# Kernel tuning notes

Measured on AMD Instinct MI355X. Metric: run time of the kernel, lower is better.

Reference implementation:

```python
import jax, jax.numpy as jnp
import numpy as np
from jax import lax

B, IN_CH, H, W = 512, 20, 32, 32
FEAT, NUM_AGENTS, NUM_ACTIONS = 128, 4, 16
NUM_UNIT, NUM_CITY = 12, 4


def setup_inputs() -> dict:
    key = jax.random.key(0)
    ks = jax.random.split(key, 6)
    states = jax.random.normal(ks[0], (B, IN_CH, H, W), dtype=jnp.float32)
    labels = jax.random.randint(ks[1], (B,), 0, NUM_AGENTS, dtype=jnp.int32)
    maskings = jnp.ones((B, 1, H, W), dtype=jnp.float32)
    # get_feature params: 3x3 conv trunk (stand-in for PolicyNetwork.get_feature)
    conv_w = jax.random.normal(ks[2], (FEAT, IN_CH, 3, 3), dtype=jnp.float32) * 0.05
    conv_b = jnp.zeros((FEAT,), dtype=jnp.float32)
    # Stacked per-agent heads: index 0 = policy_net.fc1, 1.. = fc_list
    W_all = jax.random.normal(ks[3], (NUM_AGENTS, NUM_ACTIONS, FEAT), dtype=jnp.float32) * 0.05
    b_all = jax.random.normal(ks[4], (NUM_AGENTS, NUM_ACTIONS), dtype=jnp.float32) * 0.05
    return {"states": states, "labels": labels, "maskings": maskings,
            "conv_w": conv_w, "conv_b": conv_b, "W_all": W_all, "b_all": b_all}


def _get_feature(states, maskings, conv_w, conv_b):
    x = lax.conv_general_dilated(states, conv_w, (1, 1), 'SAME',
                                 dimension_numbers=('NCHW', 'OIHW', 'NCHW'))
    x = jax.nn.relu(x + conv_b[None, :, None, None])
    return x * maskings  # [B, FEAT, H, W]


def reference(states, labels, maskings, conv_w, conv_b, W_all, b_all):
    x = _get_feature(states, maskings, conv_w, conv_b)
    b, c, h, w = x.shape
    x = x.transpose(0, 2, 3, 1).reshape(b, h * w, c)  # [B, HW, C]
    # Equivalent to computing all num_agents heads then gathering by label:
    # select each sample's head weights, then one batched GEMM.
    W_sel = W_all[labels]          # [B, K, C]
    b_sel = b_all[labels]          # [B, K]
    out = jnp.einsum('bnc,bkc->bnk', x, W_sel) + b_sel[:, None, :]
    out = out.reshape(b, h, w, NUM_ACTIONS)
    return out[..., :NUM_UNIT], out[..., NUM_UNIT:]
```

## Files before the change

kernel.cpp:

```cpp
#include <hip/hip_runtime.h>
#include <hip/hip_bf16.h>
#include <stdint.h>

#define BATCH   512
#define INCH    20
#define FEAT    128
#define KACT    16
#define NUNIT   12

typedef short bf16x8 __attribute__((ext_vector_type(8)));
typedef float f32x4  __attribute__((ext_vector_type(4)));

#define BPACK_ELEMS (3*2*4*128*8)
#define WHEAD_ELEMS (4*4*4*16*8)

#define XIN_ROWS  10
#define XIN_ELEMS (XIN_ROWS*34*20 + 64)

__device__ __forceinline__ uint16_t f2bf(float f) {
    union { float f; uint32_t u; } x{f};
    uint32_t u = x.u;
    return (uint16_t)((u + 0x7FFFu + ((u >> 16) & 1u)) >> 16);
}

__device__ __forceinline__ uint32_t cvt_pk_bf16(float lo, float hi) {
    uint32_t r;
    asm("v_cvt_pk_bf16_f32 %0, %1, %2" : "=v"(r) : "v"(lo), "v"(hi));
    return r;
}

__device__ __forceinline__ void lds_barrier() {
    asm volatile("s_waitcnt lgkmcnt(0)\n\ts_barrier" ::: "memory");
}

__global__ void repack_kernel(const float* __restrict__ conv_w,
                              const float* __restrict__ W_all,
                              uint16_t* __restrict__ Bpack,
                              uint16_t* __restrict__ Whead) {
    int idx = blockIdx.x * 256 + threadIdx.x;
    if (idx < BPACK_ELEMS) {
        int j = idx & 7, t = idx >> 3;
        int f = t & 127; t >>= 7;
        int g = t & 3;   t >>= 2;
        int kk = t & 1;  int ky = t >> 1;
        int k = kk * 32 + g * 8 + j;
        float v = 0.0f;
        if (k < 60) {
            int kx = k / 20, c = k % 20;
            v = conv_w[((f * INCH + c) * 3 + ky) * 3 + kx];
        }
        Bpack[idx] = f2bf(v);
    } else if (idx < BPACK_ELEMS + WHEAD_ELEMS) {
        int i = idx - BPACK_ELEMS;
        int j = i & 7, t = i >> 3;
        int a = t & 15; t >>= 4;
        int g = t & 3;  t >>= 2;
        int kt = t & 3; int ag = t >> 2;
        int f = kt * 32 + g * 8 + j;
        Whead[i] = f2bf(W_all[(ag * KACT + a) * FEAT + f]);
    }
}

__global__ __launch_bounds__(256, 4) void fused_mfma_kernel(
    const float* __restrict__ states,
    const int*   __restrict__ labels,
    const float* __restrict__ maskings,
    const float* __restrict__ conv_b,
    const float* __restrict__ b_all,
    const uint16_t* __restrict__ Bpack,
    const uint16_t* __restrict__ Whead,
    float*       __restrict__ out)
{
    __shared__ __align__(16) uint16_t xin[XIN_ELEMS];
    __shared__ __align__(16) uint16_t xl[2 * 32 * 128];

    const int bid  = blockIdx.x;
    const int b    = bid >> 2;
    const int y0   = (bid & 3) << 3;
    const int tid  = threadIdx.x;
    const int lane = tid & 63;
    const int fq   = tid >> 6;
    const int l15  = lane & 15;
    const int g    = lane >> 4;
    const int swz  = (l15 & 7) << 4;

    for (int i = tid; i < (XIN_ELEMS * 2) / 16; i += 256)
        ((uint4*)xin)[i] = uint4{0, 0, 0, 0};
    __syncthreads();

    for (int t = 0; t < 7; ++t) {
        int i = t * 256 + tid;
        if (i < XIN_ROWS * 5 * 32) {
            int p  = i & 31;
            int tt = i >> 5;
            int cg = tt % 5;
            int r  = tt / 5;
            int y  = y0 + r - 1;
            if (y >= 0 && y < 32) {
                const float* sp = states + (size_t)b * (INCH * 1024) + cg * 4096 + y * 32 + p;
                float v0 = sp[0], v1 = sp[1024], v2 = sp[2048], v3 = sp[3072];
                uint64_t lo = cvt_pk_bf16(v0, v1);
                uint64_t hi = cvt_pk_bf16(v2, v3);
                *(uint64_t*)&xin[(r * 34 + p + 1) * 20 + cg * 4] = lo | (hi << 32);
            }
        }
    }

    const int label = labels[b];
    f32x4 cb[2];
    #pragma unroll
    for (int nt = 0; nt < 2; ++nt)
        cb[nt] = *(const f32x4*)&conv_b[fq * 32 + nt * 16 + g * 4];
    const f32x4 hb = *(const f32x4*)&b_all[label * KACT + g * 4];
    bf16x8 Wh[4];
    #pragma unroll
    for (int kt = 0; kt < 4; ++kt)
        Wh[kt] = *(const bf16x8*)&Whead[(((label * 4 + kt) * 4 + g) * 16 + l15) * 8];

    bf16x8 Wc[3][2][2];
    #pragma unroll
    for (int ky = 0; ky < 3; ++ky)
        #pragma unroll
        for (int kk = 0; kk < 2; ++kk)
            #pragma unroll
            for (int nt = 0; nt < 2; ++nt)
                Wc[ky][kk][nt] = *(const bf16x8*)
                    &Bpack[((((ky * 2 + kk) * 4 + g) * 128 + fq * 32 + nt * 16 + l15) * 8)];

    const int hoff0 = (fq * 16 + l15) * 256;
    const bool do_head = (fq < 2);

    __syncthreads();

    #pragma unroll 2
    for (int s = 0; s < 8; ++s) {
        const int y = y0 + s;

        const float m0 = maskings[(size_t)b * 1024 + y * 32 + l15];
        const float m1 = maskings[(size_t)b * 1024 + y * 32 + 16 + l15];

        f32x4 acc[2][2];
        #pragma unroll
        for (int pt = 0; pt < 2; ++pt)
            #pragma unroll
            for (int nt = 0; nt < 2; ++nt)
                acc[pt][nt] = f32x4{0.f, 0.f, 0.f, 0.f};

        __builtin_amdgcn_s_setprio(1);
        #pragma unroll
        for (int ky = 0; ky < 3; ++ky) {
            const uint64_t* a0 = (const uint64_t*)&xin[((s + ky) * 34 + l15) * 20 + g * 8];
            const uint64_t* a1 = (const uint64_t*)&xin[((s + ky) * 34 + 16 + l15) * 20 + g * 8];
            #pragma unroll
            for (int kk = 0; kk < 2; ++kk) {
                union { uint64_t u[2]; bf16x8 v; } B0, B1;
                B0.u[0] = a0[kk * 8 + 0]; B0.u[1] = a0[kk * 8 + 1];
                B1.u[0] = a1[kk * 8 + 0]; B1.u[1] = a1[kk * 8 + 1];
                #pragma unroll
                for (int nt = 0; nt < 2; ++nt) {
                    acc[0][nt] = __builtin_amdgcn_mfma_f32_16x16x32_bf16(
                        Wc[ky][kk][nt], B0.v, acc[0][nt], 0, 0, 0);
                    acc[1][nt] = __builtin_amdgcn_mfma_f32_16x16x32_bf16(
                        Wc[ky][kk][nt], B1.v, acc[1][nt], 0, 0, 0);
                }
            }
        }
        __builtin_amdgcn_s_setprio(0);

        char* xbase = (char*)xl + (s & 1) * 8192;
        #pragma unroll
        for (int pt = 0; pt < 2; ++pt) {
            const float m = pt ? m1 : m0;
            #pragma unroll
            for (int nt = 0; nt < 2; ++nt) {
                float x0 = fmaxf(acc[pt][nt][0] + cb[nt][0], 0.f) * m;
                float x1 = fmaxf(acc[pt][nt][1] + cb[nt][1], 0.f) * m;
                float x2 = fmaxf(acc[pt][nt][2] + cb[nt][2], 0.f) * m;
                float x3 = fmaxf(acc[pt][nt][3] + cb[nt][3], 0.f) * m;
                uint64_t pk = (uint64_t)cvt_pk_bf16(x0, x1)
                            | ((uint64_t)cvt_pk_bf16(x2, x3) << 32);
                const int off = (pt * 16 + l15) * 256 + fq * 64 + nt * 32 + g * 8;
                *(uint64_t*)(xbase + (off ^ swz)) = pk;
            }
        }

        lds_barrier();

        if (do_head) {
            f32x4 hacc = f32x4{0.f, 0.f, 0.f, 0.f};
            __builtin_amdgcn_s_setprio(1);
            #pragma unroll
            for (int kt = 0; kt < 4; ++kt) {
                const int off = hoff0 + kt * 64 + g * 16;
                bf16x8 bx = *(const bf16x8*)(xbase + (off ^ swz));
                hacc = __builtin_amdgcn_mfma_f32_16x16x32_bf16(Wh[kt], bx, hacc, 0, 0, 0);
            }
            __builtin_amdgcn_s_setprio(0);
            const size_t pos = (size_t)b * 1024 + y * 32 + fq * 16 + l15;
            f32x4 o = hacc + hb;
            if (g < 3) *(f32x4*)&out[pos * NUNIT + g * 4] = o;
            else       *(f32x4*)&out[(size_t)BATCH * 1024 * NUNIT + pos * 4] = o;
        }
    }
}

extern "C" void kernel_launch(void* const* d_in, const int* in_sizes, int n_in,
                              void* d_out, int out_size, void* d_ws, size_t ws_size,
                              hipStream_t stream) {
    const float* states   = (const float*)d_in[0];
    const int*   labels   = (const int*)d_in[1];
    const float* maskings = (const float*)d_in[2];
    const float* conv_w   = (const float*)d_in[3];
    const float* conv_b   = (const float*)d_in[4];
    const float* W_all    = (const float*)d_in[5];
    const float* b_all    = (const float*)d_in[6];
    float* out = (float*)d_out;

    uint16_t* Bpack = (uint16_t*)d_ws;
    uint16_t* Whead = Bpack + BPACK_ELEMS;

    repack_kernel<<<(BPACK_ELEMS + WHEAD_ELEMS + 255) / 256, 256, 0, stream>>>(
        conv_w, W_all, Bpack, Whead);
    fused_mfma_kernel<<<BATCH * 4, 256, 0, stream>>>(
        states, labels, maskings, conv_b, b_all, Bpack, Whead, out);
}
```

Before: 42.15 us.

## Process two output rows per iteration to reuse input row loads across ky taps

New measurement: 42.62 us. No clear change (+1.1%).

```diff
diff --git a/kernel.cpp b/kernel.cpp
--- a/kernel.cpp
+++ b/kernel.cpp
@@ -61,7 +61,7 @@
     }
 }
 
-__global__ __launch_bounds__(256, 4) void fused_mfma_kernel(
+__global__ __launch_bounds__(256, 3) void fused_mfma_kernel(
     const float* __restrict__ states,
     const int*   __restrict__ labels,
     const float* __restrict__ maskings,
@@ -72,7 +72,7 @@
     float*       __restrict__ out)
 {
     __shared__ __align__(16) uint16_t xin[XIN_ELEMS];
-    __shared__ __align__(16) uint16_t xl[2 * 32 * 128];
+    __shared__ __align__(16) uint16_t xl[2 * 64 * 128];
 
     const int bid  = blockIdx.x;
     const int b    = bid >> 2;
@@ -128,65 +128,74 @@
                     &Bpack[((((ky * 2 + kk) * 4 + g) * 128 + fq * 32 + nt * 16 + l15) * 8)];
 
     const int hoff0 = (fq * 16 + l15) * 256;
-    const bool do_head = (fq < 2);
 
     __syncthreads();
 
     #pragma unroll 2
-    for (int s = 0; s < 8; ++s) {
-        const int y = y0 + s;
-
-        const float m0 = maskings[(size_t)b * 1024 + y * 32 + l15];
-        const float m1 = maskings[(size_t)b * 1024 + y * 32 + 16 + l15];
-
-        f32x4 acc[2][2];
+    for (int s = 0; s < 4; ++s) {
+        float mk[2][2];
         #pragma unroll
-        for (int pt = 0; pt < 2; ++pt)
-            #pragma unroll
-            for (int nt = 0; nt < 2; ++nt)
-                acc[pt][nt] = f32x4{0.f, 0.f, 0.f, 0.f};
+        for (int rr = 0; rr < 2; ++rr)
+            #pragma unroll
+            for (int pt = 0; pt < 2; ++pt)
+                mk[rr][pt] = maskings[(size_t)b * 1024 + (y0 + 2 * s + rr) * 32 + pt * 16 + l15];
+
+        char* xbase = (char*)xl + (s & 1) * 16384;
 
         __builtin_amdgcn_s_setprio(1);
         #pragma unroll
-        for (int ky = 0; ky < 3; ++ky) {
-            const uint64_t* a0 = (const uint64_t*)&xin[((s + ky) * 34 + l15) * 20 + g * 8];
-            const uint64_t* a1 = (const uint64_t*)&xin[((s + ky) * 34 + 16 + l15) * 20 + g * 8];
-            #pragma unroll
-            for (int kk = 0; kk < 2; ++kk) {
-                union { uint64_t u[2]; bf16x8 v; } B0, B1;
-                B0.u[0] = a0[kk * 8 + 0]; B0.u[1] = a0[kk * 8 + 1];
-                B1.u[0] = a1[kk * 8 + 0]; B1.u[1] = a1[kk * 8 + 1];
+        for (int pt = 0; pt < 2; ++pt) {
+            f32x4 a0[2], a1[2];
+            #pragma unroll
+            for (int nt = 0; nt < 2; ++nt) {
+                a0[nt] = f32x4{0.f, 0.f, 0.f, 0.f};
+                a1[nt] = f32x4{0.f, 0.f, 0.f, 0.f};
+            }
+
+            #pragma unroll
+            for (int t = 0; t < 4; ++t) {
+                const uint64_t* ap = (const uint64_t*)
+                    &xin[((2 * s + t) * 34 + pt * 16 + l15) * 20 + g * 8];
+                union { uint64_t u[2]; bf16x8 v; } X0, X1;
+                X0.u[0] = ap[0]; X0.u[1] = ap[1];
+                X1.u[0] = ap[8]; X1.u[1] = ap[9];
+                #pragma unroll
+                for (int kk = 0; kk < 2; ++kk) {
+                    const bf16x8 Xk = kk ? X1.v : X0.v;
+                    #pragma unroll
+                    for (int nt = 0; nt < 2; ++nt) {
+                        if (t < 3)
+                            a0[nt] = __builtin_amdgcn_mfma_f32_16x16x32_bf16(
+                                Wc[t][kk][nt], Xk, a0[nt], 0, 0, 0);
+                        if (t > 0)
+                            a1[nt] = __builtin_amdgcn_mfma_f32_16x16x32_bf16(
+                                Wc[t - 1][kk][nt], Xk, a1[nt], 0, 0, 0);
+                    }
+                }
+            }
+
+            #pragma unroll
+            for (int rr = 0; rr < 2; ++rr) {
+                const float m = mk[rr][pt];
                 #pragma unroll
                 for (int nt = 0; nt < 2; ++nt) {
-                    acc[0][nt] = __builtin_amdgcn_mfma_f32_16x16x32_bf16(
-                        Wc[ky][kk][nt], B0.v, acc[0][nt], 0, 0, 0);
-                    acc[1][nt] = __builtin_amdgcn_mfma_f32_16x16x32_bf16(
-                        Wc[ky][kk][nt], B1.v, acc[1][nt], 0, 0, 0);
+                    const f32x4 A = rr ? a1[nt] : a0[nt];
+                    float x0 = fmaxf(A[0] + cb[nt][0], 0.f) * m;
+                    float x1 = fmaxf(A[1] + cb[nt][1], 0.f) * m;
+                    float x2 = fmaxf(A[2] + cb[nt][2], 0.f) * m;
+                    float x3 = fmaxf(A[3] + cb[nt][3], 0.f) * m;
+                    uint64_t pk = (uint64_t)cvt_pk_bf16(x0, x1)
+                                | ((uint64_t)cvt_pk_bf16(x2, x3) << 32);
+                    const int off = ((rr * 2 + pt) * 16 + l15) * 256 + fq * 64 + nt * 32 + g * 8;
+                    *(uint64_t*)(xbase + (off ^ swz)) = pk;
                 }
             }
         }
         __builtin_amdgcn_s_setprio(0);
 
-        char* xbase = (char*)xl + (s & 1) * 8192;
-        #pragma unroll
-        for (int pt = 0; pt < 2; ++pt) {
-            const float m = pt ? m1 : m0;
-            #pragma unroll
-            for (int nt = 0; nt < 2; ++nt) {
-                float x0 = fmaxf(acc[pt][nt][0] + cb[nt][0], 0.f) * m;
-                float x1 = fmaxf(acc[pt][nt][1] + cb[nt][1], 0.f) * m;
-                float x2 = fmaxf(acc[pt][nt][2] + cb[nt][2], 0.f) * m;
-                float x3 = fmaxf(acc[pt][nt][3] + cb[nt][3], 0.f) * m;
-                uint64_t pk = (uint64_t)cvt_pk_bf16(x0, x1)
-                            | ((uint64_t)cvt_pk_bf16(x2, x3) << 32);
-                const int off = (pt * 16 + l15) * 256 + fq * 64 + nt * 32 + g * 8;
-                *(uint64_t*)(xbase + (off ^ swz)) = pk;
-            }
-        }
-
         lds_barrier();
 
-        if (do_head) {
+        {
             f32x4 hacc = f32x4{0.f, 0.f, 0.f, 0.f};
             __builtin_amdgcn_s_setprio(1);
             #pragma unroll
@@ -196,7 +205,8 @@
                 hacc = __builtin_amdgcn_mfma_f32_16x16x32_bf16(Wh[kt], bx, hacc, 0, 0, 0);
             }
             __builtin_amdgcn_s_setprio(0);
-            const size_t pos = (size_t)b * 1024 + y * 32 + fq * 16 + l15;
+            const int y = y0 + 2 * s + (fq >> 1);
+            const size_t pos = (size_t)b * 1024 + y * 32 + (fq & 1) * 16 + l15;
             f32x4 o = hacc + hb;
             if (g < 3) *(f32x4*)&out[pos * NUNIT + g * 4] = o;
             else       *(f32x4*)&out[(size_t)BATCH * 1024 * NUNIT + pos * 4] = o;
```
